# Optimization experiments

Measured on AMD Instinct MI355X. Metric: run time of the kernel, lower is better.

The kernel has to match this reference:

```python
import jax, jax.numpy as jnp
import numpy as np

WEIGHT = 1e-9
SIGMA_RGB = 15.0
SIGMA_XY = 100.0
SCALE = 0.5  # downscale factor (integer stride 2)


def _down_nearest(x):
    # PyTorch F.interpolate(mode='nearest', scale_factor=0.5): out[i]=in[2i]
    return x[..., ::2, ::2]


def _down_bilinear2(x):
    # PyTorch bilinear, align_corners=False, scale 0.5: src = 2i + 0.5
    # -> average of the 2x2 input block (exact, no antialiasing).
    N, K, H, W = x.shape
    return x.reshape(N, K, H // 2, 2, W // 2, 2).mean(axis=(3, 5))


def setup_inputs() -> dict:
    key = jax.random.key(0)
    k1, k2, k3 = jax.random.split(key, 3)
    N, K, H, W = 8, 21, 128, 128
    images = jax.random.uniform(k1, (N, 3, H, W), jnp.float32) * 255.0
    logS = jax.random.normal(k2, (N, K, H, W), jnp.float32)
    log1_S = jax.random.normal(k3, (N, K, H, W), jnp.float32)
    ROIs = jnp.ones((N, H, W), jnp.float32)
    return {"images": images, "logS": logS, "log1_S": log1_S, "ROIs": ROIs}


def reference(images, logS, log1_S, ROIs):
    # 1) downscale all inputs (scale_factor = 0.5)
    img = _down_nearest(images)            # [N,3,h,w]
    lS = _down_bilinear2(logS)             # [N,K,h,w]
    l1S = _down_bilinear2(log1_S)          # [N,K,h,w]
    roi = _down_nearest(ROIs)              # [N,h,w]

    N, K, h, w = lS.shape
    P = h * w
    sxy = SIGMA_XY * SCALE

    # bilateral features: (r,g,b)/sigma_rgb ++ (x,y)/sigma_xy
    yy, xx = jnp.meshgrid(jnp.arange(h, dtype=jnp.float32),
                          jnp.arange(w, dtype=jnp.float32), indexing='ij')
    feat_pos = jnp.stack([xx, yy], axis=-1).reshape(P, 2) / sxy          # [P,2]
    feat_rgb = (img / SIGMA_RGB).transpose(0, 2, 3, 1).reshape(N, P, 3)  # [N,P,3]
    feats = jnp.concatenate(
        [feat_rgb, jnp.broadcast_to(feat_pos, (N, P, 2))], axis=-1)      # [N,P,5]

    # ROI masking (applied to both logS and log(1-S), as in the torch code)
    roi_f = roi.reshape(N, 1, P)
    lS_m = lS.reshape(N, K, P) * roi_f
    l1S_m = l1S.reshape(N, K, P) * roi_f

    def per_image(f, a, b):
        # dense Gaussian bilateral kernel W_pq = exp(-0.5 ||f_p - f_q||^2)
        sq = jnp.sum(f * f, axis=-1)                      # [P]
        d2 = sq[:, None] + sq[None, :] - 2.0 * (f @ f.T)  # [P,P]
        Wk = jnp.exp(-0.5 * d2)
        Ab = jnp.einsum('pq,kq->kp', Wk, b)               # W @ log(1-S)
        return jnp.sum(a * Ab)                            # logS . (W log(1-S))

    losses = jax.vmap(per_image)(feats, lS_m, l1S_m)      # [N]
    return WEIGHT * jnp.sum(losses) / N
```

## Files before the change

kernel.cpp:

```cpp
#include <hip/hip_runtime.h>

#define NIMG 8
#define KCH 21
#define HW2 16384
#define PD 4096
#define NT 256
#define RT 4
#define SQRT_LOG2E 1.2011224087864498f

typedef __attribute__((ext_vector_type(8))) short short8;
typedef __attribute__((ext_vector_type(4))) float f32x4;

__device__ __forceinline__ unsigned short bf16rne(float x) {
    unsigned u = __float_as_uint(x);
    unsigned r = (u + 0x7FFFu + ((u >> 16) & 1u)) >> 16;
    return (unsigned short)r;
}
__device__ __forceinline__ float bf2f(unsigned short b) {
    return __uint_as_float(((unsigned)b) << 16);
}

__global__ __launch_bounds__(256)
void prep_ab(const float* __restrict__ logS, const float* __restrict__ log1S,
             const float* __restrict__ rois,
             unsigned short* __restrict__ AopM, unsigned short* __restrict__ BopM)
{
    unsigned u = blockIdx.x * 256 + threadIdx.x;
    int p  = u & 4095;
    int nk = u >> 12;
    int n  = nk / KCH;
    int k  = nk - n * KCH;
    int i = p >> 6, j = p & 63;
    int base = (i << 8) + (j << 1);

    float roi = rois[n * HW2 + base];
    const float* ls = logS  + (size_t)nk * HW2;
    const float* l1 = log1S + (size_t)nk * HW2;
    float a = 0.25f * (ls[base] + ls[base+1] + ls[base+128] + ls[base+129]) * roi;
    float b = 0.25f * (l1[base] + l1[base+1] + l1[base+128] + l1[base+129]) * roi;

    size_t t = (size_t)((n * NT + (p >> 4)) * 4 + (k >> 3)) * 128 + (p & 15) * 8 + (k & 7);
    AopM[t] = bf16rne(a);
    BopM[t] = bf16rne(b);
}

__global__ __launch_bounds__(256)
void prep_feat(const float* __restrict__ images,
               unsigned short* __restrict__ GA, unsigned short* __restrict__ GB,
               float* __restrict__ Hh)
{
    int t = blockIdx.x * 256 + threadIdx.x;
    int n = t >> 12, p = t & 4095;
    int i = p >> 6, j = p & 63;
    int base = (i << 8) + (j << 1);
    const float* img = images + (size_t)n * 3 * HW2;

    float f[5];
    f[0] = img[base]          * (SQRT_LOG2E / 15.0f);
    f[1] = img[HW2 + base]    * (SQRT_LOG2E / 15.0f);
    f[2] = img[2*HW2 + base]  * (SQRT_LOG2E / 15.0f);
    f[3] = (float)j * (SQRT_LOG2E / 50.0f);
    f[4] = (float)i * (SQRT_LOG2E / 50.0f);

    unsigned short hi[5], lo[5];
    float h = 0.0f;
#pragma unroll
    for (int c = 0; c < 5; ++c) {
        hi[c] = bf16rne(f[c]);
        float hf = bf2f(hi[c]);
        lo[c] = bf16rne(f[c] - hf);
        float fh = hf + bf2f(lo[c]);
        h = fmaf(fh, fh, h);
    }
    Hh[t] = 0.5f * h;

    int rt = p >> 4, m = p & 15;
    unsigned short* ga = GA + (size_t)(n * NT + rt) * 512 + m * 8;
    unsigned short* gb = GB + (size_t)(n * NT + rt) * 512 + m * 8;

    unsigned short av[32], bv[32];
#pragma unroll
    for (int s = 0; s < 32; ++s) {
        unsigned short a = 0, b = 0;
        if      (s < 5)  { a = hi[s];      b = hi[s];      }
        else if (s < 10) { a = hi[s - 5];  b = lo[s - 5];  }
        else if (s < 15) { a = lo[s - 10]; b = hi[s - 10]; }
        else if (s < 20) { a = lo[s - 15]; b = lo[s - 15]; }
        av[s] = a; bv[s] = b;
    }
#pragma unroll
    for (int g = 0; g < 4; ++g)
#pragma unroll
        for (int e2 = 0; e2 < 4; ++e2) {
            int s = g * 8 + e2 * 2;
            ushort2 pa; pa.x = av[s]; pa.y = av[s + 1];
            ushort2 pb; pb.x = bv[s]; pb.y = bv[s + 1];
            *reinterpret_cast<ushort2*>(ga + g * 128 + e2 * 2) = pa;
            *reinterpret_cast<ushort2*>(gb + g * 128 + e2 * 2) = pb;
        }
}

__global__ __launch_bounds__(256)
void crf_kernel(const unsigned short* __restrict__ AopM,
                const unsigned short* __restrict__ BopM,
                const unsigned short* __restrict__ GA,
                const unsigned short* __restrict__ GB,
                const float* __restrict__ Hh,
                float* __restrict__ partials)
{
    const int tid = threadIdx.x;
    const int l = tid & 63;
    const int w = __builtin_amdgcn_readfirstlane(tid >> 6);
    const int unit = blockIdx.x * 4 + w;
    const int n = unit >> 9;
    const int rem = unit & 511;
    const int rt0 = (rem >> 3) << 2;
    const int seg = rem & 7;

    const int lf  = l * 8;
    const int lq  = l & 15;
    const int lr4 = (l >> 4) << 2;

    short8 aM[RT], aG[RT];
    float hp[RT][4];
    const float* hb = Hh + n * PD;
#pragma unroll
    for (int i = 0; i < RT; ++i) {
        const size_t tb = (size_t)(n * NT + rt0 + i) * 512;
        aM[i] = *reinterpret_cast<const short8*>(AopM + tb + lf);
        aG[i] = *reinterpret_cast<const short8*>(GA   + tb + lf);
        float4 h4 = *reinterpret_cast<const float4*>(hb + (rt0 + i) * 16 + lr4);
        hp[i][0] = h4.x; hp[i][1] = h4.y; hp[i][2] = h4.z; hp[i][3] = h4.w;
    }

    const int ct0 = seg * 32;
    const unsigned short* bMb = BopM + (size_t)(n * NT + ct0) * 512;
    const unsigned short* bGb = GB   + (size_t)(n * NT + ct0) * 512;
    const float* hqb = hb + ct0 * 16;

    const f32x4 zero = {0.0f, 0.0f, 0.0f, 0.0f};
    float acc[RT] = {0.0f, 0.0f, 0.0f, 0.0f};

    short8 bm = *reinterpret_cast<const short8*>(bMb + lf);
    short8 bg = *reinterpret_cast<const short8*>(bGb + lf);
    float  hq = hqb[lq];

#pragma unroll 4
    for (int tt = 0; tt < 32; ++tt) {
        const int nx = (tt + 1 < 32) ? tt + 1 : 31;
        short8 bm_n = *reinterpret_cast<const short8*>(bMb + nx * 512 + lf);
        short8 bg_n = *reinterpret_cast<const short8*>(bGb + nx * 512 + lf);
        float  hq_n = hqb[nx * 16 + lq];

#pragma unroll
        for (int i = 0; i < RT; ++i) {
            f32x4 mm = __builtin_amdgcn_mfma_f32_16x16x32_bf16(aM[i], bm, zero, 0, 0, 0);
            f32x4 gg = __builtin_amdgcn_mfma_f32_16x16x32_bf16(aG[i], bg, zero, 0, 0, 0);
#pragma unroll
            for (int r = 0; r < 4; ++r) {
                float e2 = gg[r] - (hp[i][r] + hq);
                float wgt;
                asm("v_exp_f32 %0, %1" : "=v"(wgt) : "v"(e2));
                acc[i] = fmaf(wgt, mm[r], acc[i]);
            }
        }
        bm = bm_n; bg = bg_n; hq = hq_n;
    }

    float partial = (acc[0] + acc[1]) + (acc[2] + acc[3]);
#pragma unroll
    for (int off = 32; off; off >>= 1)
        partial += __shfl_down(partial, off, 64);

    __shared__ float sred[4];
    if (l == 0) sred[w] = partial;
    __syncthreads();
    if (tid == 0)
        partials[blockIdx.x] = (sred[0] + sred[1]) + (sred[2] + sred[3]);
}

__global__ __launch_bounds__(256)
void reduce_kernel(const float* __restrict__ partials, float* __restrict__ out, int count)
{
    __shared__ float s[256];
    float sum = 0.0f;
    for (int i = threadIdx.x; i < count; i += 256) sum += partials[i];
    s[threadIdx.x] = sum;
    __syncthreads();
    for (int st = 128; st > 0; st >>= 1) {
        if (threadIdx.x < st) s[threadIdx.x] += s[threadIdx.x + st];
        __syncthreads();
    }
    if (threadIdx.x == 0) out[0] = s[0] * (1e-9f / 8.0f);
}

extern "C" void kernel_launch(void* const* d_in, const int* in_sizes, int n_in,
                              void* d_out, int out_size, void* d_ws, size_t ws_size,
                              hipStream_t stream)
{
    const float* images = (const float*)d_in[0];
    const float* logS   = (const float*)d_in[1];
    const float* log1S  = (const float*)d_in[2];
    const float* rois   = (const float*)d_in[3];
    float* out = (float*)d_out;

    unsigned short* AopM = (unsigned short*)d_ws;
    unsigned short* BopM = AopM + (1u << 20);
    unsigned short* GA   = BopM + (1u << 20);
    unsigned short* GB   = GA   + (1u << 20);
    float* Hh            = (float*)(GB + (1u << 20));
    float* partials      = Hh + NIMG * PD;

    hipMemsetAsync(AopM, 0, (size_t)(1u << 21) * sizeof(unsigned short), stream);

    prep_ab<<<2688, 256, 0, stream>>>(logS, log1S, rois, AopM, BopM);
    prep_feat<<<128, 256, 0, stream>>>(images, GA, GB, Hh);
    crf_kernel<<<1024, 256, 0, stream>>>(AopM, BopM, GA, GB, Hh, partials);
    reduce_kernel<<<1, 256, 0, stream>>>(partials, out, 1024);
}
```

Baseline: 117.6 us.

## Fold squared-norm terms into MFMA operands and merge prep kernels

```diff
diff --git a/kernel.cpp b/kernel.cpp
--- a/kernel.cpp
+++ b/kernel.cpp
@@ -21,83 +21,98 @@
 }
 
 __global__ __launch_bounds__(256)
-void prep_ab(const float* __restrict__ logS, const float* __restrict__ log1S,
-             const float* __restrict__ rois,
-             unsigned short* __restrict__ AopM, unsigned short* __restrict__ BopM)
-{
-    unsigned u = blockIdx.x * 256 + threadIdx.x;
-    int p  = u & 4095;
-    int nk = u >> 12;
-    int n  = nk / KCH;
-    int k  = nk - n * KCH;
-    int i = p >> 6, j = p & 63;
-    int base = (i << 8) + (j << 1);
-
-    float roi = rois[n * HW2 + base];
-    const float* ls = logS  + (size_t)nk * HW2;
-    const float* l1 = log1S + (size_t)nk * HW2;
-    float a = 0.25f * (ls[base] + ls[base+1] + ls[base+128] + ls[base+129]) * roi;
-    float b = 0.25f * (l1[base] + l1[base+1] + l1[base+128] + l1[base+129]) * roi;
-
-    size_t t = (size_t)((n * NT + (p >> 4)) * 4 + (k >> 3)) * 128 + (p & 15) * 8 + (k & 7);
-    AopM[t] = bf16rne(a);
-    BopM[t] = bf16rne(b);
-}
-
-__global__ __launch_bounds__(256)
-void prep_feat(const float* __restrict__ images,
-               unsigned short* __restrict__ GA, unsigned short* __restrict__ GB,
-               float* __restrict__ Hh)
-{
-    int t = blockIdx.x * 256 + threadIdx.x;
-    int n = t >> 12, p = t & 4095;
-    int i = p >> 6, j = p & 63;
-    int base = (i << 8) + (j << 1);
-    const float* img = images + (size_t)n * 3 * HW2;
-
-    float f[5];
-    f[0] = img[base]          * (SQRT_LOG2E / 15.0f);
-    f[1] = img[HW2 + base]    * (SQRT_LOG2E / 15.0f);
-    f[2] = img[2*HW2 + base]  * (SQRT_LOG2E / 15.0f);
-    f[3] = (float)j * (SQRT_LOG2E / 50.0f);
-    f[4] = (float)i * (SQRT_LOG2E / 50.0f);
-
-    unsigned short hi[5], lo[5];
-    float h = 0.0f;
-#pragma unroll
-    for (int c = 0; c < 5; ++c) {
-        hi[c] = bf16rne(f[c]);
-        float hf = bf2f(hi[c]);
-        lo[c] = bf16rne(f[c] - hf);
-        float fh = hf + bf2f(lo[c]);
-        h = fmaf(fh, fh, h);
-    }
-    Hh[t] = 0.5f * h;
-
-    int rt = p >> 4, m = p & 15;
-    unsigned short* ga = GA + (size_t)(n * NT + rt) * 512 + m * 8;
-    unsigned short* gb = GB + (size_t)(n * NT + rt) * 512 + m * 8;
-
-    unsigned short av[32], bv[32];
-#pragma unroll
-    for (int s = 0; s < 32; ++s) {
-        unsigned short a = 0, b = 0;
-        if      (s < 5)  { a = hi[s];      b = hi[s];      }
-        else if (s < 10) { a = hi[s - 5];  b = lo[s - 5];  }
-        else if (s < 15) { a = lo[s - 10]; b = hi[s - 10]; }
-        else if (s < 20) { a = lo[s - 15]; b = lo[s - 15]; }
-        av[s] = a; bv[s] = b;
-    }
-#pragma unroll
-    for (int g = 0; g < 4; ++g)
-#pragma unroll
-        for (int e2 = 0; e2 < 4; ++e2) {
-            int s = g * 8 + e2 * 2;
-            ushort2 pa; pa.x = av[s]; pa.y = av[s + 1];
-            ushort2 pb; pb.x = bv[s]; pb.y = bv[s + 1];
-            *reinterpret_cast<ushort2*>(ga + g * 128 + e2 * 2) = pa;
-            *reinterpret_cast<ushort2*>(gb + g * 128 + e2 * 2) = pb;
-        }
+void prep_kernel(const float* __restrict__ images,
+                 const float* __restrict__ logS, const float* __restrict__ log1S,
+                 const float* __restrict__ rois,
+                 unsigned short* __restrict__ AopM, unsigned short* __restrict__ BopM,
+                 unsigned short* __restrict__ GA, unsigned short* __restrict__ GB)
+{
+    const int bid = blockIdx.x;
+    if (bid < 2048) {
+        unsigned t = bid * 256 + threadIdx.x;
+        int h = t & 2047;
+        int k = (t >> 11) & 31;
+        int n = t >> 16;
+        int p0 = h << 1;
+        size_t o = (size_t)((n * NT + (p0 >> 4)) * 4 + (k >> 3)) * 128
+                 + (p0 & 15) * 8 + (k & 7);
+        unsigned short a0 = 0, a1 = 0, b0 = 0, b1 = 0;
+        if (k < KCH) {
+            int i = p0 >> 6, j0 = p0 & 63;
+            int base = (i << 8) + (j0 << 1);
+            int nk = n * KCH + k;
+            const float* ls = logS  + (size_t)nk * HW2;
+            const float* l1 = log1S + (size_t)nk * HW2;
+            float4 lsa = *reinterpret_cast<const float4*>(ls + base);
+            float4 lsb = *reinterpret_cast<const float4*>(ls + base + 128);
+            float4 l1a = *reinterpret_cast<const float4*>(l1 + base);
+            float4 l1b = *reinterpret_cast<const float4*>(l1 + base + 128);
+            float4 rr  = *reinterpret_cast<const float4*>(rois + (size_t)n * HW2 + base);
+            a0 = bf16rne(0.25f * (lsa.x + lsa.y + lsb.x + lsb.y) * rr.x);
+            a1 = bf16rne(0.25f * (lsa.z + lsa.w + lsb.z + lsb.w) * rr.z);
+            b0 = bf16rne(0.25f * (l1a.x + l1a.y + l1b.x + l1b.y) * rr.x);
+            b1 = bf16rne(0.25f * (l1a.z + l1a.w + l1b.z + l1b.w) * rr.z);
+        }
+        AopM[o] = a0; AopM[o + 8] = a1;
+        BopM[o] = b0; BopM[o + 8] = b1;
+    } else {
+        int t = (bid - 2048) * 256 + threadIdx.x;
+        int n = t >> 12, p = t & 4095;
+        int i = p >> 6, j = p & 63;
+        int base = (i << 8) + (j << 1);
+        const float* img = images + (size_t)n * 3 * HW2;
+
+        float f[5];
+        f[0] = img[base]           * (SQRT_LOG2E / 15.0f);
+        f[1] = img[HW2 + base]     * (SQRT_LOG2E / 15.0f);
+        f[2] = img[2 * HW2 + base] * (SQRT_LOG2E / 15.0f);
+        f[3] = (float)j * (SQRT_LOG2E / 50.0f);
+        f[4] = (float)i * (SQRT_LOG2E / 50.0f);
+
+        unsigned short hi[5], lo[5];
+        float hsum = 0.0f;
+#pragma unroll
+        for (int c = 0; c < 5; ++c) {
+            hi[c] = bf16rne(f[c]);
+            float hf = bf2f(hi[c]);
+            lo[c] = bf16rne(f[c] - hf);
+            float fh = hf + bf2f(lo[c]);
+            hsum = fmaf(fh, fh, hsum);
+        }
+        float nh = -0.5f * hsum;
+        unsigned short nhh = bf16rne(nh);
+        unsigned short nhl = bf16rne(nh - bf2f(nhh));
+        const unsigned short one = 0x3F80;
+
+        unsigned short av[32], bv[32];
+#pragma unroll
+        for (int s = 0; s < 32; ++s) { av[s] = 0; bv[s] = 0; }
+#pragma unroll
+        for (int c = 0; c < 5; ++c) {
+            av[c]      = hi[c]; bv[c]      = hi[c];
+            av[c + 5]  = hi[c]; bv[c + 5]  = lo[c];
+            av[c + 10] = lo[c]; bv[c + 10] = hi[c];
+            av[c + 15] = lo[c]; bv[c + 15] = lo[c];
+        }
+        av[20] = nhh; bv[20] = one;
+        av[21] = nhl; bv[21] = one;
+        av[22] = one; bv[22] = nhh;
+        av[23] = one; bv[23] = nhl;
+
+        int rt = p >> 4, m = p & 15;
+        unsigned short* ga = GA + (size_t)(n * NT + rt) * 512 + m * 8;
+        unsigned short* gb = GB + (size_t)(n * NT + rt) * 512 + m * 8;
+#pragma unroll
+        for (int g = 0; g < 4; ++g)
+#pragma unroll
+            for (int e2 = 0; e2 < 4; ++e2) {
+                int s = g * 8 + e2 * 2;
+                ushort2 pa; pa.x = av[s]; pa.y = av[s + 1];
+                ushort2 pb; pb.x = bv[s]; pb.y = bv[s + 1];
+                *reinterpret_cast<ushort2*>(ga + g * 128 + e2 * 2) = pa;
+                *reinterpret_cast<ushort2*>(gb + g * 128 + e2 * 2) = pb;
+            }
+    }
 }
 
 __global__ __launch_bounds__(256)
@@ -105,7 +120,6 @@
                 const unsigned short* __restrict__ BopM,
                 const unsigned short* __restrict__ GA,
                 const unsigned short* __restrict__ GB,
-                const float* __restrict__ Hh,
                 float* __restrict__ partials)
 {
     const int tid = threadIdx.x;
@@ -116,41 +130,31 @@
     const int rem = unit & 511;
     const int rt0 = (rem >> 3) << 2;
     const int seg = rem & 7;
-
-    const int lf  = l * 8;
-    const int lq  = l & 15;
-    const int lr4 = (l >> 4) << 2;
+    const int lf = l * 8;
 
     short8 aM[RT], aG[RT];
-    float hp[RT][4];
-    const float* hb = Hh + n * PD;
 #pragma unroll
     for (int i = 0; i < RT; ++i) {
         const size_t tb = (size_t)(n * NT + rt0 + i) * 512;
         aM[i] = *reinterpret_cast<const short8*>(AopM + tb + lf);
         aG[i] = *reinterpret_cast<const short8*>(GA   + tb + lf);
-        float4 h4 = *reinterpret_cast<const float4*>(hb + (rt0 + i) * 16 + lr4);
-        hp[i][0] = h4.x; hp[i][1] = h4.y; hp[i][2] = h4.z; hp[i][3] = h4.w;
     }
 
     const int ct0 = seg * 32;
     const unsigned short* bMb = BopM + (size_t)(n * NT + ct0) * 512;
     const unsigned short* bGb = GB   + (size_t)(n * NT + ct0) * 512;
-    const float* hqb = hb + ct0 * 16;
 
     const f32x4 zero = {0.0f, 0.0f, 0.0f, 0.0f};
     float acc[RT] = {0.0f, 0.0f, 0.0f, 0.0f};
 
     short8 bm = *reinterpret_cast<const short8*>(bMb + lf);
     short8 bg = *reinterpret_cast<const short8*>(bGb + lf);
-    float  hq = hqb[lq];
 
 #pragma unroll 4
     for (int tt = 0; tt < 32; ++tt) {
         const int nx = (tt + 1 < 32) ? tt + 1 : 31;
         short8 bm_n = *reinterpret_cast<const short8*>(bMb + nx * 512 + lf);
         short8 bg_n = *reinterpret_cast<const short8*>(bGb + nx * 512 + lf);
-        float  hq_n = hqb[nx * 16 + lq];
 
 #pragma unroll
         for (int i = 0; i < RT; ++i) {
@@ -158,13 +162,12 @@
             f32x4 gg = __builtin_amdgcn_mfma_f32_16x16x32_bf16(aG[i], bg, zero, 0, 0, 0);
 #pragma unroll
             for (int r = 0; r < 4; ++r) {
-                float e2 = gg[r] - (hp[i][r] + hq);
                 float wgt;
-                asm("v_exp_f32 %0, %1" : "=v"(wgt) : "v"(e2));
+                asm("v_exp_f32 %0, %1" : "=v"(wgt) : "v"(gg[r]));
                 acc[i] = fmaf(wgt, mm[r], acc[i]);
             }
         }
-        bm = bm_n; bg = bg_n; hq = hq_n;
+        bm = bm_n; bg = bg_n;
     }
 
     float partial = (acc[0] + acc[1]) + (acc[2] + acc[3]);
@@ -208,13 +211,10 @@
     unsigned short* BopM = AopM + (1u << 20);
     unsigned short* GA   = BopM + (1u << 20);
     unsigned short* GB   = GA   + (1u << 20);
-    float* Hh            = (float*)(GB + (1u << 20));
-    float* partials      = Hh + NIMG * PD;
-
-    hipMemsetAsync(AopM, 0, (size_t)(1u << 21) * sizeof(unsigned short), stream);
-
-    prep_ab<<<2688, 256, 0, stream>>>(logS, log1S, rois, AopM, BopM);
-    prep_feat<<<128, 256, 0, stream>>>(images, GA, GB, Hh);
-    crf_kernel<<<1024, 256, 0, stream>>>(AopM, BopM, GA, GB, Hh, partials);
+    float* partials      = (float*)(GB + (1u << 20));
+
+    prep_kernel<<<2176, 256, 0, stream>>>(images, logS, log1S, rois,
+                                          AopM, BopM, GA, GB);
+    crf_kernel<<<1024, 256, 0, stream>>>(AopM, BopM, GA, GB, partials);
     reduce_kernel<<<1, 256, 0, stream>>>(partials, out, 1024);
 }
```

Measured after the change: 109.8 us. 6.7% less time.
